# Kernel tuning notes

Measured on AMD Instinct MI355X. Metric: run time of the kernel, lower is better.

## Reference

```python
import jax, jax.numpy as jnp
import numpy as np

N_NODES = 100000
N_EDGES = 3200000
D_IN = 128
D_OUT = 128


def setup_inputs() -> dict:
    key = jax.random.key(0)
    k1, k2, k3, k4, k5, k6 = jax.random.split(key, 6)
    x = jax.random.normal(k1, (N_NODES, D_IN), dtype=jnp.float32)
    edge_row = jnp.sort(jax.random.randint(k2, (N_EDGES,), 0, N_NODES, dtype=jnp.int32))
    edge_col = jax.random.randint(k3, (N_EDGES,), 0, N_NODES, dtype=jnp.int32)
    edge_val = jax.random.uniform(k4, (N_EDGES,), dtype=jnp.float32)
    stdv = 1.0 / np.sqrt(D_OUT)
    weight = jax.random.uniform(k5, (D_IN, D_OUT), dtype=jnp.float32, minval=-stdv, maxval=stdv)
    bias = jax.random.uniform(k6, (D_OUT,), dtype=jnp.float32, minval=-stdv, maxval=stdv)
    return {"x": x, "edge_row": edge_row, "edge_col": edge_col,
            "edge_val": edge_val, "weight": weight, "bias": bias}


def reference(x, edge_row, edge_col, edge_val, weight, bias):
    # support = A @ x  (sparse COO SpMM via gather + segment-sum scatter)
    gathered = x[edge_col] * edge_val[:, None]          # [E, D_IN]
    support = jax.ops.segment_sum(gathered, edge_row, num_segments=N_NODES)  # [N, D_IN]
    # output = support @ W + b
    return support @ weight + bias
```

## Files before the change

kernel.cpp:

```cpp
#include <hip/hip_runtime.h>

#define NNODES 100000
#define NEDGES 3200000
#define DIM    128

typedef __bf16  bf16x8 __attribute__((ext_vector_type(8)));
typedef unsigned short u16;
typedef u16     u16x8  __attribute__((ext_vector_type(8)));
typedef float   f32x4  __attribute__((ext_vector_type(4)));
typedef float   f32x2  __attribute__((ext_vector_type(2)));
typedef unsigned int u32;

__device__ __forceinline__ u16 f2bf(float f) {
    union { float f; unsigned int i; } c;
    c.f = f;
    unsigned int x = c.i;
    unsigned int rounding = 0x7fff + ((x >> 16) & 1);
    x += rounding;
    return (u16)(x >> 16);
}

__device__ __forceinline__ float asf(u32 u) {
    union { u32 i; float f; } c; c.i = u; return c.f;
}

__device__ __forceinline__ bf16x8 ldfrag_u16(const u16* p) {
    u16x8 u = *(const u16x8*)p;
    return __builtin_bit_cast(bf16x8, u);
}

__device__ __forceinline__ bf16x8 ldfrag_f32(const float* p) {
    f32x4 a = *(const f32x4*)p;
    f32x4 b = *(const f32x4*)(p + 4);
    u16x8 u;
#pragma unroll
    for (int i = 0; i < 4; ++i) u[i] = f2bf(a[i]);
#pragma unroll
    for (int i = 0; i < 4; ++i) u[4 + i] = f2bf(b[i]);
    return __builtin_bit_cast(bf16x8, u);
}

__global__ void build_row_ptr(const int* __restrict__ edge_row,
                              int* __restrict__ row_ptr) {
    int n = blockIdx.x * blockDim.x + threadIdx.x;
    if (n > NNODES) return;
    int lo = 0, hi = NEDGES;
    while (lo < hi) {
        int mid = (lo + hi) >> 1;
        if (edge_row[mid] < n) lo = mid + 1; else hi = mid;
    }
    row_ptr[n] = lo;
}

__global__ void prep_wt(const float* __restrict__ w, u16* __restrict__ wt) {
    int i = blockIdx.x * blockDim.x + threadIdx.x;
    if (i >= DIM * DIM) return;
    int k = i >> 7, n = i & 127;
    wt[n * DIM + k] = f2bf(w[k * DIM + n]);
}

#define WT_STRIDE 136
__global__ __launch_bounds__(256) void gemm_xw(const float* __restrict__ x,
                                               const u16* __restrict__ wt,
                                               u16* __restrict__ y) {
    __shared__ u16 wlds[DIM * WT_STRIDE];
    __shared__ u16 ybounce[4][16 * DIM];

    int tid = threadIdx.x;
    {
        const f32x4* src = (const f32x4*)wt;
#pragma unroll
        for (int i = 0; i < 8; ++i) {
            int ci  = tid + 256 * i;
            int row = ci >> 4, off = ci & 15;
            *((f32x4*)(wlds + row * WT_STRIDE) + off) = src[ci];
        }
    }
    __syncthreads();

    int wave = __builtin_amdgcn_readfirstlane(tid >> 6);
    int lane = tid & 63;
    int quad = lane >> 4, l16 = lane & 15;
    int mBase = (blockIdx.x * 4 + wave) * 16;
    if (mBase >= NNODES) return;

    const float* xrow = x + (size_t)(mBase + l16) * DIM + quad * 8;

    f32x4 acc[8];
#pragma unroll
    for (int nt = 0; nt < 8; ++nt) acc[nt] = (f32x4){0.f, 0.f, 0.f, 0.f};

#pragma unroll
    for (int kb = 0; kb < 4; ++kb) {
        bf16x8 a = ldfrag_f32(xrow + kb * 32);
#pragma unroll
        for (int nt = 0; nt < 8; ++nt) {
            bf16x8 b = ldfrag_u16(wlds + (nt * 16 + l16) * WT_STRIDE + kb * 32 + quad * 8);
            acc[nt] = __builtin_amdgcn_mfma_f32_16x16x32_bf16(a, b, acc[nt], 0, 0, 0);
        }
    }

    u16* yb = ybounce[wave];
#pragma unroll
    for (int nt = 0; nt < 8; ++nt) {
        int col = nt * 16 + l16;
#pragma unroll
        for (int r = 0; r < 4; ++r)
            yb[(quad * 4 + r) * DIM + col] = f2bf(acc[nt][r]);
    }
#pragma unroll
    for (int j = 0; j < 4; ++j) {
        int lr = j * 4 + quad;
        u16x8 t = *(const u16x8*)(yb + lr * DIM + l16 * 8);
        *(u16x8*)(y + (size_t)(mBase + lr) * DIM + l16 * 8) = t;
    }
}

__global__ __launch_bounds__(256) void spmm(const int* __restrict__ row_ptr,
                                            const int* __restrict__ ecol,
                                            const float* __restrict__ eval,
                                            const u16* __restrict__ y,
                                            const float* __restrict__ bias,
                                            float* __restrict__ out) {
    int lane = threadIdx.x & 63;
    int row  = __builtin_amdgcn_readfirstlane(blockIdx.x * 4 + (threadIdx.x >> 6));
    if (row >= NNODES) return;

    int lo = row_ptr[row];
    int hi = row_ptr[row + 1];

    const u16* yl = y + lane * 2;
    float acc0 = 0.f, acc1 = 0.f;

    int e = lo;
    for (; e + 8 <= hi; e += 8) {
        int c[8]; float v[8];
#pragma unroll
        for (int s = 0; s < 8; ++s) { c[s] = ecol[e + s]; v[s] = eval[e + s]; }
        u32 p[8];
#pragma unroll
        for (int s = 0; s < 8; ++s) p[s] = *(const u32*)(yl + (size_t)c[s] * DIM);
#pragma unroll
        for (int s = 0; s < 8; ++s) {
            acc0 += v[s] * asf(p[s] << 16);
            acc1 += v[s] * asf(p[s] & 0xffff0000u);
        }
    }
    for (; e + 4 <= hi; e += 4) {
        int c[4]; float v[4];
#pragma unroll
        for (int s = 0; s < 4; ++s) { c[s] = ecol[e + s]; v[s] = eval[e + s]; }
        u32 p[4];
#pragma unroll
        for (int s = 0; s < 4; ++s) p[s] = *(const u32*)(yl + (size_t)c[s] * DIM);
#pragma unroll
        for (int s = 0; s < 4; ++s) {
            acc0 += v[s] * asf(p[s] << 16);
            acc1 += v[s] * asf(p[s] & 0xffff0000u);
        }
    }
    for (; e < hi; ++e) {
        int   c = ecol[e];
        float v = eval[e];
        u32   p = *(const u32*)(yl + (size_t)c * DIM);
        acc0 += v * asf(p << 16);
        acc1 += v * asf(p & 0xffff0000u);
    }

    f32x2 o;
    o[0] = acc0 + bias[lane * 2];
    o[1] = acc1 + bias[lane * 2 + 1];
    __builtin_nontemporal_store(o, (f32x2*)(out + (size_t)row * DIM + lane * 2));
}

extern "C" void kernel_launch(void* const* d_in, const int* in_sizes, int n_in,
                              void* d_out, int out_size, void* d_ws, size_t ws_size,
                              hipStream_t stream) {
    const float* x        = (const float*)d_in[0];
    const int*   edge_row = (const int*)d_in[1];
    const int*   edge_col = (const int*)d_in[2];
    const float* edge_val = (const float*)d_in[3];
    const float* weight   = (const float*)d_in[4];
    const float* bias     = (const float*)d_in[5];
    float* out = (float*)d_out;

    char* ws = (char*)d_ws;
    u16* y       = (u16*)ws;
    int* row_ptr = (int*)(ws + (size_t)NNODES * DIM * 2);
    u16* wt      = (u16*)(ws + 26000128);

    prep_wt<<<(DIM * DIM + 255) / 256, 256, 0, stream>>>(weight, wt);
    build_row_ptr<<<(NNODES + 1 + 255) / 256, 256, 0, stream>>>(edge_row, row_ptr);

    gemm_xw<<<(NNODES / 16 + 3) / 4, 256, 0, stream>>>(x, wt, y);

    spmm<<<NNODES / 4, 256, 0, stream>>>(row_ptr, edge_col, edge_val, y, bias, out);
}
```

Before: 248.8 us.

## Split SpMM wave into four edge groups with 16-byte row gathers

The SpMM kernel now splits each wave into four 16-lane groups. Each group handles a different edge at the same time, and each lane gathers 8 bf16 values with one 16-byte load instead of one 4-byte load per lane. The partial sums from the four groups are combined with xor shuffles, and one group writes the result with vector stores. Edges are taken 16 at a time; the leftover edges go through a masked 4-wide tail that sets the weight to zero for invalid slots. A launch-bounds occupancy hint is also added. The aim is to cut the number of gather instructions and keep more bytes in flight per load. The cost is extra shuffle reduction work, more registers per lane, and idle lanes on the writeback.

```diff
diff --git a/kernel.cpp b/kernel.cpp
--- a/kernel.cpp
+++ b/kernel.cpp
@@ -8,8 +8,8 @@
 typedef unsigned short u16;
 typedef u16     u16x8  __attribute__((ext_vector_type(8)));
 typedef float   f32x4  __attribute__((ext_vector_type(4)));
-typedef float   f32x2  __attribute__((ext_vector_type(2)));
 typedef unsigned int u32;
+typedef u32     u32x4  __attribute__((ext_vector_type(4)));
 
 __device__ __forceinline__ u16 f2bf(float f) {
     union { float f; unsigned int i; } c;
@@ -116,12 +116,12 @@
     }
 }
 
-__global__ __launch_bounds__(256) void spmm(const int* __restrict__ row_ptr,
-                                            const int* __restrict__ ecol,
-                                            const float* __restrict__ eval,
-                                            const u16* __restrict__ y,
-                                            const float* __restrict__ bias,
-                                            float* __restrict__ out) {
+__global__ __launch_bounds__(256, 8) void spmm(const int* __restrict__ row_ptr,
+                                               const int* __restrict__ ecol,
+                                               const float* __restrict__ eval,
+                                               const u16* __restrict__ y,
+                                               const float* __restrict__ bias,
+                                               float* __restrict__ out) {
     int lane = threadIdx.x & 63;
     int row  = __builtin_amdgcn_readfirstlane(blockIdx.x * 4 + (threadIdx.x >> 6));
     if (row >= NNODES) return;
@@ -129,48 +129,67 @@
     int lo = row_ptr[row];
     int hi = row_ptr[row + 1];
 
-    const u16* yl = y + lane * 2;
-    float acc0 = 0.f, acc1 = 0.f;
+    int grp = lane >> 4;
+    int sub = lane & 15;
+
+    float acc[8];
+#pragma unroll
+    for (int j = 0; j < 8; ++j) acc[j] = 0.f;
+
+    const u16* ychunk = y + sub * 8;
 
     int e = lo;
-    for (; e + 8 <= hi; e += 8) {
-        int c[8]; float v[8];
-#pragma unroll
-        for (int s = 0; s < 8; ++s) { c[s] = ecol[e + s]; v[s] = eval[e + s]; }
-        u32 p[8];
-#pragma unroll
-        for (int s = 0; s < 8; ++s) p[s] = *(const u32*)(yl + (size_t)c[s] * DIM);
-#pragma unroll
-        for (int s = 0; s < 8; ++s) {
-            acc0 += v[s] * asf(p[s] << 16);
-            acc1 += v[s] * asf(p[s] & 0xffff0000u);
-        }
-    }
-    for (; e + 4 <= hi; e += 4) {
-        int c[4]; float v[4];
-#pragma unroll
-        for (int s = 0; s < 4; ++s) { c[s] = ecol[e + s]; v[s] = eval[e + s]; }
-        u32 p[4];
-#pragma unroll
-        for (int s = 0; s < 4; ++s) p[s] = *(const u32*)(yl + (size_t)c[s] * DIM);
-#pragma unroll
-        for (int s = 0; s < 4; ++s) {
-            acc0 += v[s] * asf(p[s] << 16);
-            acc1 += v[s] * asf(p[s] & 0xffff0000u);
-        }
-    }
-    for (; e < hi; ++e) {
-        int   c = ecol[e];
-        float v = eval[e];
-        u32   p = *(const u32*)(yl + (size_t)c * DIM);
-        acc0 += v * asf(p << 16);
-        acc1 += v * asf(p & 0xffff0000u);
-    }
-
-    f32x2 o;
-    o[0] = acc0 + bias[lane * 2];
-    o[1] = acc1 + bias[lane * 2 + 1];
-    __builtin_nontemporal_store(o, (f32x2*)(out + (size_t)row * DIM + lane * 2));
+    for (; e + 16 <= hi; e += 16) {
+#pragma unroll
+        for (int b = 0; b < 4; ++b) {
+            int e0 = e + b * 4;
+            int   c0 = ecol[e0], c1 = ecol[e0 + 1], c2 = ecol[e0 + 2], c3 = ecol[e0 + 3];
+            float v0 = eval[e0], v1 = eval[e0 + 1], v2 = eval[e0 + 2], v3 = eval[e0 + 3];
+            int   c = grp < 2 ? (grp == 0 ? c0 : c1) : (grp == 2 ? c2 : c3);
+            float v = grp < 2 ? (grp == 0 ? v0 : v1) : (grp == 2 ? v2 : v3);
+            u32x4 q = *(const u32x4*)(ychunk + (size_t)c * DIM);
+#pragma unroll
+            for (int j = 0; j < 4; ++j) {
+                acc[2 * j]     += v * asf(q[j] << 16);
+                acc[2 * j + 1] += v * asf(q[j] & 0xffff0000u);
+            }
+        }
+    }
+    for (; e < hi; e += 4) {
+        int rem = hi - e;
+        int i1 = rem > 1 ? e + 1 : e, i2 = rem > 2 ? e + 2 : e, i3 = rem > 3 ? e + 3 : e;
+        int   c0 = ecol[e],  c1 = ecol[i1], c2 = ecol[i2], c3 = ecol[i3];
+        float v0 = eval[e];
+        float v1 = rem > 1 ? eval[i1] : 0.f;
+        float v2 = rem > 2 ? eval[i2] : 0.f;
+        float v3 = rem > 3 ? eval[i3] : 0.f;
+        int   c = grp < 2 ? (grp == 0 ? c0 : c1) : (grp == 2 ? c2 : c3);
+        float v = grp < 2 ? (grp == 0 ? v0 : v1) : (grp == 2 ? v2 : v3);
+        u32x4 q = *(const u32x4*)(ychunk + (size_t)c * DIM);
+#pragma unroll
+        for (int j = 0; j < 4; ++j) {
+            acc[2 * j]     += v * asf(q[j] << 16);
+            acc[2 * j + 1] += v * asf(q[j] & 0xffff0000u);
+        }
+    }
+
+#pragma unroll
+    for (int j = 0; j < 8; ++j) {
+        acc[j] += __shfl_xor(acc[j], 16);
+        acc[j] += __shfl_xor(acc[j], 32);
+    }
+
+    if (grp == 0) {
+        float* orow = out + (size_t)row * DIM + sub * 8;
+        f32x4 o0, o1;
+#pragma unroll
+        for (int j = 0; j < 4; ++j) {
+            o0[j] = acc[j]     + bias[sub * 8 + j];
+            o1[j] = acc[4 + j] + bias[sub * 8 + 4 + j];
+        }
+        __builtin_nontemporal_store(o0, (f32x4*)orow);
+        __builtin_nontemporal_store(o1, (f32x4*)(orow + 4));
+    }
 }
 
 extern "C" void kernel_launch(void* const* d_in, const int* in_sizes, int n_in,
```

Result: no change. 246.1 us (-1.1%).
